# Performance work log

Hardware: AMD Instinct MI355X
Metric: run time of the kernel (lower is better)

Reference implementation:

```python
import jax, jax.numpy as jnp
import numpy as np

TOP_K = 2  # routing_method: renormalize top-2 (topk then softmax over selected logits)


def setup_inputs() -> dict:
    key = jax.random.key(0)
    ks = jax.random.split(key, 5)
    T, H, I, E = 4096, 1024, 4096, 8
    return {
        "hidden_states": jax.random.normal(ks[0], (T, H), jnp.float32),
        "router_logits": jax.random.normal(ks[1], (T, E), jnp.float32),
        "W_gate": jax.random.normal(ks[2], (E, H, I), jnp.float32) * 0.02,  # w1
        "W_up": jax.random.normal(ks[3], (E, H, I), jnp.float32) * 0.02,   # w3
        "W_down": jax.random.normal(ks[4], (E, I, H), jnp.float32) * 0.02, # w2
    }


def reference(hidden_states, router_logits, W_gate, W_up, W_down):
    # Routing: top-k logits, renormalize with softmax over selected logits.
    top_vals, top_idx = jax.lax.top_k(router_logits, TOP_K)        # [T, K]
    routing_weights = jax.nn.softmax(top_vals, axis=-1)            # [T, K]

    E = W_gate.shape[0]
    out = jnp.zeros_like(hidden_states)                            # [T, H]
    for e in range(E):  # fixed small expert loop (structurally distinct weights)
        # combine weight for expert e per token (0 if not routed here)
        w_e = jnp.sum(jnp.where(top_idx == e, routing_weights, 0.0), axis=-1)  # [T]
        gate = hidden_states @ W_gate[e]                           # [T, I]
        up = hidden_states @ W_up[e]                               # [T, I]
        y = (jax.nn.silu(gate) * up) @ W_down[e]                   # [T, H]
        out = out + w_e[:, None] * y
    return out
```

## Files before the change

### kernel.cpp

```cpp
#include <hip/hip_runtime.h>

typedef float    f32x4 __attribute__((ext_vector_type(4)));
typedef _Float16 f16x8 __attribute__((ext_vector_type(8)));
typedef _Float16 f16x4 __attribute__((ext_vector_type(4)));

#define T_TOK 4096
#define HD    1024
#define ID    4096
#define NE    8
#define TOTP  (2*T_TOK)
#define BM    128
#define BN    128
#define MAXTILES 72

#define WS_CNT   0
#define WS_FILL  64
#define WS_OFF   128
#define WS_TOT   192
#define WS_TEXP  256
#define WS_TM0   (256 + 4*MAXTILES)
#define WS_TOPE  1024
#define WS_TOPW  (WS_TOPE + 4*TOTP)
#define WS_PAIR  (WS_TOPW + 4*TOTP)
#define WS_ACT   ((size_t)1 << 20)
constexpr size_t WS_YBUF = WS_ACT  + 2ull*TOTP*ID;
constexpr size_t WS_HS16 = WS_YBUF + 2ull*TOTP*HD;
constexpr size_t WS_WG16 = WS_HS16 + 2ull*T_TOK*HD;
constexpr size_t WS_WU16 = WS_WG16 + 2ull*NE*HD*ID;
constexpr size_t WS_WD16 = WS_WU16 + 2ull*NE*HD*ID;

__device__ __forceinline__ void gll16(const void* g, void* l) {
  __builtin_amdgcn_global_load_lds(
      (const __attribute__((address_space(1))) unsigned int*)g,
      (__attribute__((address_space(3))) unsigned int*)l, 16, 0, 0);
}

#define WAITV(N) do { \
    asm volatile("s_waitcnt vmcnt(" #N ")" ::: "memory"); \
    __builtin_amdgcn_sched_barrier(0); \
  } while (0)

__device__ __forceinline__ int lofs(int row, int g) {
  return row * 32 + ((g ^ ((row >> 1) & 3)) << 3);
}

__global__ void k_router(const float* __restrict__ logits, char* __restrict__ ws) {
  int t = blockIdx.x * blockDim.x + threadIdx.x;
  if (t >= T_TOK) return;
  float v0 = -1e30f, v1 = -1e30f; int i0 = 0, i1 = 0;
  #pragma unroll
  for (int e = 0; e < NE; ++e) {
    float v = logits[t * NE + e];
    if (v > v0)      { v1 = v0; i1 = i0; v0 = v; i0 = e; }
    else if (v > v1) { v1 = v;  i1 = e; }
  }
  float w0 = 1.f / (1.f + __expf(v1 - v0));
  ((int*)(ws + WS_TOPE))[2*t]   = i0;
  ((int*)(ws + WS_TOPE))[2*t+1] = i1;
  ((float*)(ws + WS_TOPW))[2*t]   = w0;
  ((float*)(ws + WS_TOPW))[2*t+1] = 1.f - w0;
  atomicAdd(&((int*)(ws + WS_CNT))[i0], 1);
  atomicAdd(&((int*)(ws + WS_CNT))[i1], 1);
}

__global__ void k_prefix(char* __restrict__ ws) {
  if (threadIdx.x != 0 || blockIdx.x != 0) return;
  const int* cnt = (const int*)(ws + WS_CNT);
  int* off  = (int*)(ws + WS_OFF);
  int* texp = (int*)(ws + WS_TEXP);
  int* tm0  = (int*)(ws + WS_TM0);
  int run = 0, tiles = 0;
  for (int e = 0; e < NE; ++e) {
    off[e] = run;
    int ne = cnt[e];
    for (int i = 0; i < ne; i += BM) { texp[tiles] = e; tm0[tiles] = i; ++tiles; }
    run += ne;
  }
  off[NE] = run;
  *(int*)(ws + WS_TOT) = tiles;
}

__global__ void k_scatter(char* __restrict__ ws) {
  int t = blockIdx.x * blockDim.x + threadIdx.x;
  if (t >= T_TOK) return;
  const int* tope = (const int*)(ws + WS_TOPE);
  const int* off  = (const int*)(ws + WS_OFF);
  int* fill = (int*)(ws + WS_FILL);
  int* pair = (int*)(ws + WS_PAIR);
  #pragma unroll
  for (int s = 0; s < 2; ++s) {
    int id = 2*t + s;
    int e = tope[id];
    int pos = off[e] + atomicAdd(&fill[e], 1);
    pair[pos] = id;
  }
}

__global__ void k_hscvt(const float* __restrict__ src, _Float16* __restrict__ dst) {
  int i = blockIdx.x * blockDim.x + threadIdx.x;
  f32x4 v = ((const f32x4*)src)[i];
  f16x4 o;
  #pragma unroll
  for (int j = 0; j < 4; ++j) o[j] = (_Float16)v[j];
  ((f16x4*)dst)[i] = o;
}

__global__ __launch_bounds__(256) void k_wtrans(const float* __restrict__ src,
                                                _Float16* __restrict__ dst,
                                                int K, int N) {
  const int e = blockIdx.z;
  const int n0 = blockIdx.x * 64, k0 = blockIdx.y * 64;
  const float* s = src + (size_t)e * K * N;
  _Float16* d = dst + (size_t)e * (size_t)K * N;
  __shared__ _Float16 t[64][68];
  const int tx = threadIdx.x & 15, ty = threadIdx.x >> 4;
  #pragma unroll
  for (int it = 0; it < 4; ++it) {
    int k = k0 + it*16 + ty;
    f32x4 v = *(const f32x4*)&s[(size_t)k * N + n0 + tx*4];
    #pragma unroll
    for (int j = 0; j < 4; ++j) t[tx*4 + j][it*16 + ty] = (_Float16)v[j];
  }
  __syncthreads();
  #pragma unroll
  for (int it = 0; it < 4; ++it) {
    int n = it*16 + ty;
    *(f16x4*)&d[(size_t)(n0 + n) * K + k0 + tx*4] = *(const f16x4*)&t[n][tx*4];
  }
}

__global__ __launch_bounds__(512) void k_gemm1(
    const _Float16* __restrict__ hs16, const _Float16* __restrict__ WgT,
    const _Float16* __restrict__ WuT, char* __restrict__ ws) {
  const int s = blockIdx.y;
  if (s >= *(const int*)(ws + WS_TOT)) return;
  const int e    = ((const int*)(ws + WS_TEXP))[s];
  const int m0   = ((const int*)(ws + WS_TM0))[s];
  const int offE = ((const int*)(ws + WS_OFF))[e];
  const int nE   = ((const int*)(ws + WS_CNT))[e];
  _Float16* __restrict__ act = (_Float16*)(ws + WS_ACT);
  const int n0 = blockIdx.x * BN;
  const int tid = threadIdx.x, lane = tid & 63, wid = tid >> 6;

  __shared__ __align__(16) _Float16 sm[3 * 3 * BM * 32];

  const int rL = lane >> 2;
  const int q  = (((lane & 3) ^ ((lane >> 3) & 3)) << 3);
  int tok;
  { int mm = m0 + 16*wid + rL;
    tok = (mm < nE) ? (((const int*)(ws + WS_PAIR))[offE + mm] >> 1) : 0; }
  const _Float16* aS = hs16 + (size_t)tok * HD + q;
  const int colB = n0 + 16*wid + rL;
  const _Float16* gS = WgT + ((size_t)e * ID + colB) * HD + q;
  const _Float16* uS = WuT + ((size_t)e * ID + colB) * HD + q;

  auto stage = [&](int buf, int kt) {
    _Float16* b = sm + buf * (3*BM*32) + wid * 512;
    const int ko = kt * 32;
    gll16(aS + ko, b);
    gll16(gS + ko, b + BM*32);
    gll16(uS + ko, b + 2*BM*32);
  };

  const int wr = wid >> 2, wc = wid & 3;
  const int l15 = lane & 15, l4 = lane >> 4;
  f32x4 accg[4][2] = {}, accu[4][2] = {};

  auto compute = [&](int buf) {
    const _Float16* b0 = sm + buf * (3*BM*32);
    f16x8 afr[4], gfr[2], ufr[2];
    #pragma unroll
    for (int i = 0; i < 4; ++i)
      afr[i] = *(const f16x8*)&b0[lofs(64*wr + 16*i + l15, l4)];
    #pragma unroll
    for (int j = 0; j < 2; ++j) {
      gfr[j] = *(const f16x8*)&b0[BM*32   + lofs(32*wc + 16*j + l15, l4)];
      ufr[j] = *(const f16x8*)&b0[2*BM*32 + lofs(32*wc + 16*j + l15, l4)];
    }
    __builtin_amdgcn_s_setprio(1);
    #pragma unroll
    for (int i = 0; i < 4; ++i)
      #pragma unroll
      for (int j = 0; j < 2; ++j) {
        accg[i][j] = __builtin_amdgcn_mfma_f32_16x16x32_f16(afr[i], gfr[j], accg[i][j], 0, 0, 0);
        accu[i][j] = __builtin_amdgcn_mfma_f32_16x16x32_f16(afr[i], ufr[j], accu[i][j], 0, 0, 0);
      }
    __builtin_amdgcn_s_setprio(0);
  };

  const int KT = HD / 32;
  stage(0, 0); stage(1, 1);
  for (int t = 0; t < KT - 2; ++t) {
    stage((t + 2) % 3, t + 2);
    WAITV(6);
    __builtin_amdgcn_s_barrier();
    compute(t % 3);
    __builtin_amdgcn_s_barrier();
  }
  WAITV(3);
  __builtin_amdgcn_s_barrier();
  compute((KT - 2) % 3);
  __builtin_amdgcn_s_barrier();
  WAITV(0);
  __builtin_amdgcn_s_barrier();
  compute((KT - 1) % 3);

  #pragma unroll
  for (int i = 0; i < 4; ++i)
    #pragma unroll
    for (int r = 0; r < 4; ++r) {
      const int mm = m0 + 64*wr + 16*i + 4*l4 + r;
      if (mm < nE) {
        const size_t prow = (size_t)(offE + mm) * ID;
        #pragma unroll
        for (int j = 0; j < 2; ++j) {
          float g = accg[i][j][r], u = accu[i][j][r];
          float sv = g / (1.f + __expf(-g)) * u;
          act[prow + n0 + 32*wc + 16*j + l15] = (_Float16)sv;
        }
      }
    }
}

__global__ __launch_bounds__(512) void k_gemm2(const _Float16* __restrict__ WdT,
                                               char* __restrict__ ws) {
  const int s = blockIdx.y;
  if (s >= *(const int*)(ws + WS_TOT)) return;
  const int e    = ((const int*)(ws + WS_TEXP))[s];
  const int m0   = ((const int*)(ws + WS_TM0))[s];
  const int offE = ((const int*)(ws + WS_OFF))[e];
  const int nE   = ((const int*)(ws + WS_CNT))[e];
  const int* __restrict__ pair = (const int*)(ws + WS_PAIR);
  const _Float16* __restrict__ act = (const _Float16*)(ws + WS_ACT);
  _Float16* __restrict__ ybuf = (_Float16*)(ws + WS_YBUF);
  const int n0 = blockIdx.x * BN;
  const int tid = threadIdx.x, lane = tid & 63, wid = tid >> 6;

  __shared__ __align__(16) _Float16 sm[3 * 2 * BM * 32];

  const int rL = lane >> 2;
  const int q  = (((lane & 3) ^ ((lane >> 3) & 3)) << 3);
  int pA; { int mm = m0 + 16*wid + rL; pA = (mm < nE) ? (offE + mm) : 0; }
  const _Float16* aS = act + (size_t)pA * ID + q;
  const int cB = n0 + 16*wid + rL;
  const _Float16* bS = WdT + ((size_t)e * HD + cB) * ID + q;

  auto stage = [&](int buf, int kt) {
    _Float16* b = sm + buf * (2*BM*32) + wid * 512;
    const int ko = kt * 32;
    gll16(aS + ko, b);
    gll16(bS + ko, b + BM*32);
  };

  const int wr = wid >> 2, wc = wid & 3;
  const int l15 = lane & 15, l4 = lane >> 4;
  f32x4 acc[4][2] = {};

  auto compute = [&](int buf) {
    const _Float16* b0 = sm + buf * (2*BM*32);
    f16x8 afr[4], bfr[2];
    #pragma unroll
    for (int i = 0; i < 4; ++i)
      afr[i] = *(const f16x8*)&b0[lofs(64*wr + 16*i + l15, l4)];
    #pragma unroll
    for (int j = 0; j < 2; ++j)
      bfr[j] = *(const f16x8*)&b0[BM*32 + lofs(32*wc + 16*j + l15, l4)];
    __builtin_amdgcn_s_setprio(1);
    #pragma unroll
    for (int i = 0; i < 4; ++i)
      #pragma unroll
      for (int j = 0; j < 2; ++j)
        acc[i][j] = __builtin_amdgcn_mfma_f32_16x16x32_f16(afr[i], bfr[j], acc[i][j], 0, 0, 0);
    __builtin_amdgcn_s_setprio(0);
  };

  const int KT = ID / 32;
  stage(0, 0); stage(1, 1);
  for (int t = 0; t < KT - 2; ++t) {
    stage((t + 2) % 3, t + 2);
    WAITV(4);
    __builtin_amdgcn_s_barrier();
    compute(t % 3);
    __builtin_amdgcn_s_barrier();
  }
  WAITV(2);
  __builtin_amdgcn_s_barrier();
  compute((KT - 2) % 3);
  __builtin_amdgcn_s_barrier();
  WAITV(0);
  __builtin_amdgcn_s_barrier();
  compute((KT - 1) % 3);

  #pragma unroll
  for (int i = 0; i < 4; ++i)
    #pragma unroll
    for (int r = 0; r < 4; ++r) {
      const int mm = m0 + 64*wr + 16*i + 4*l4 + r;
      if (mm < nE) {
        const int id = pair[offE + mm];
        #pragma unroll
        for (int j = 0; j < 2; ++j)
          ybuf[(size_t)id * HD + n0 + 32*wc + 16*j + l15] = (_Float16)acc[i][j][r];
      }
    }
}

__global__ void k_combine(const char* __restrict__ ws, float* __restrict__ out) {
  const int idx = blockIdx.x * blockDim.x + threadIdx.x;
  const int t = idx >> 7, c = idx & 127;
  const float* topw = (const float*)(ws + WS_TOPW);
  const _Float16* yb = (const _Float16*)(ws + WS_YBUF);
  f16x8 y0 = ((const f16x8*)(yb + (size_t)(2*t)     * HD))[c];
  f16x8 y1 = ((const f16x8*)(yb + (size_t)(2*t + 1) * HD))[c];
  const float w0 = topw[2*t], w1 = topw[2*t+1];
  f32x4 o0, o1;
  #pragma unroll
  for (int j = 0; j < 4; ++j) {
    o0[j] = w0 * (float)y0[j]     + w1 * (float)y1[j];
    o1[j] = w0 * (float)y0[4 + j] + w1 * (float)y1[4 + j];
  }
  ((f32x4*)out)[2*idx]     = o0;
  ((f32x4*)out)[2*idx + 1] = o1;
}

extern "C" void kernel_launch(void* const* d_in, const int* in_sizes, int n_in,
                              void* d_out, int out_size, void* d_ws, size_t ws_size,
                              hipStream_t stream) {
  const float* hs     = (const float*)d_in[0];
  const float* logits = (const float*)d_in[1];
  const float* Wg     = (const float*)d_in[2];
  const float* Wu     = (const float*)d_in[3];
  const float* Wd     = (const float*)d_in[4];
  char* ws = (char*)d_ws;

  _Float16* hs16 = (_Float16*)(ws + WS_HS16);
  _Float16* wg16 = (_Float16*)(ws + WS_WG16);
  _Float16* wu16 = (_Float16*)(ws + WS_WU16);
  _Float16* wd16 = (_Float16*)(ws + WS_WD16);

  hipMemsetAsync(ws, 0, 256, stream);
  k_router <<<dim3(T_TOK/256), dim3(256), 0, stream>>>(logits, ws);
  k_prefix <<<dim3(1),         dim3(64),  0, stream>>>(ws);
  k_scatter<<<dim3(T_TOK/256), dim3(256), 0, stream>>>(ws);
  k_hscvt  <<<dim3(T_TOK*HD/4/256), dim3(256), 0, stream>>>(hs, hs16);
  k_wtrans <<<dim3(ID/64, HD/64, NE), dim3(256), 0, stream>>>(Wg, wg16, HD, ID);
  k_wtrans <<<dim3(ID/64, HD/64, NE), dim3(256), 0, stream>>>(Wu, wu16, HD, ID);
  k_wtrans <<<dim3(HD/64, ID/64, NE), dim3(256), 0, stream>>>(Wd, wd16, ID, HD);
  k_gemm1  <<<dim3(ID/BN, MAXTILES), dim3(512), 0, stream>>>(hs16, wg16, wu16, ws);
  k_gemm2  <<<dim3(HD/BN, MAXTILES), dim3(512), 0, stream>>>(wd16, ws);
  k_combine<<<dim3(T_TOK*HD/8/256), dim3(256), 0, stream>>>(ws, (float*)d_out);
}
```

Before: 490.3 us.

## Enlarge GEMM block tiles to 128x256 and 256x128 with split staging

The gate/up GEMM now computes a 128x256 output tile per block, processing gate and up sequentially with a shared B-fragment register set. The down GEMM uses 256-row token tiles over 128 columns, with a separate tile list built in the prefix kernel. Each loop iteration issues part of its loads before the barrier and the rest after it, to spread out global-to-LDS traffic. Larger tiles raise arithmetic intensity and cut re-reads of weights and activations, but they use more LDS and registers per block and give fewer blocks for the MoE-sized workload.

```diff
diff --git a/kernel.cpp b/kernel.cpp
--- a/kernel.cpp
+++ b/kernel.cpp
@@ -9,17 +9,19 @@
 #define ID    4096
 #define NE    8
 #define TOTP  (2*T_TOK)
-#define BM    128
-#define BN    128
-#define MAXTILES 72
+#define MAXT1 72
+#define MAXT2 40
 
 #define WS_CNT   0
 #define WS_FILL  64
 #define WS_OFF   128
 #define WS_TOT   192
+#define WS_TOT2  196
 #define WS_TEXP  256
-#define WS_TM0   (256 + 4*MAXTILES)
-#define WS_TOPE  1024
+#define WS_TM0   (256 + 4*MAXT1)
+#define WS_TEXP2 (256 + 8*MAXT1)
+#define WS_TM02  (256 + 8*MAXT1 + 4*MAXT2)
+#define WS_TOPE  2048
 #define WS_TOPW  (WS_TOPE + 4*TOTP)
 #define WS_PAIR  (WS_TOPW + 4*TOTP)
 #define WS_ACT   ((size_t)1 << 20)
@@ -66,18 +68,22 @@
 __global__ void k_prefix(char* __restrict__ ws) {
   if (threadIdx.x != 0 || blockIdx.x != 0) return;
   const int* cnt = (const int*)(ws + WS_CNT);
-  int* off  = (int*)(ws + WS_OFF);
-  int* texp = (int*)(ws + WS_TEXP);
-  int* tm0  = (int*)(ws + WS_TM0);
-  int run = 0, tiles = 0;
+  int* off   = (int*)(ws + WS_OFF);
+  int* texp  = (int*)(ws + WS_TEXP);
+  int* tm0   = (int*)(ws + WS_TM0);
+  int* texp2 = (int*)(ws + WS_TEXP2);
+  int* tm02  = (int*)(ws + WS_TM02);
+  int run = 0, t1 = 0, t2 = 0;
   for (int e = 0; e < NE; ++e) {
     off[e] = run;
     int ne = cnt[e];
-    for (int i = 0; i < ne; i += BM) { texp[tiles] = e; tm0[tiles] = i; ++tiles; }
+    for (int i = 0; i < ne; i += 128) { texp[t1] = e; tm0[t1] = i; ++t1; }
+    for (int i = 0; i < ne; i += 256) { texp2[t2] = e; tm02[t2] = i; ++t2; }
     run += ne;
   }
   off[NE] = run;
-  *(int*)(ws + WS_TOT) = tiles;
+  *(int*)(ws + WS_TOT)  = t1;
+  *(int*)(ws + WS_TOT2) = t2;
 }
 
 __global__ void k_scatter(char* __restrict__ ws) {
@@ -129,6 +135,7 @@
   }
 }
 
+#define G1_BUF 20480
 __global__ __launch_bounds__(512) void k_gemm1(
     const _Float16* __restrict__ hs16, const _Float16* __restrict__ WgT,
     const _Float16* __restrict__ WuT, char* __restrict__ ws) {
@@ -139,65 +146,82 @@
   const int offE = ((const int*)(ws + WS_OFF))[e];
   const int nE   = ((const int*)(ws + WS_CNT))[e];
   _Float16* __restrict__ act = (_Float16*)(ws + WS_ACT);
-  const int n0 = blockIdx.x * BN;
+  const int n0 = blockIdx.x * 256;
   const int tid = threadIdx.x, lane = tid & 63, wid = tid >> 6;
 
-  __shared__ __align__(16) _Float16 sm[3 * 3 * BM * 32];
+  __shared__ __align__(16) _Float16 sm[3 * G1_BUF];
 
   const int rL = lane >> 2;
   const int q  = (((lane & 3) ^ ((lane >> 3) & 3)) << 3);
   int tok;
   { int mm = m0 + 16*wid + rL;
     tok = (mm < nE) ? (((const int*)(ws + WS_PAIR))[offE + mm] >> 1) : 0; }
-  const _Float16* aS = hs16 + (size_t)tok * HD + q;
-  const int colB = n0 + 16*wid + rL;
-  const _Float16* gS = WgT + ((size_t)e * ID + colB) * HD + q;
-  const _Float16* uS = WuT + ((size_t)e * ID + colB) * HD + q;
-
-  auto stage = [&](int buf, int kt) {
-    _Float16* b = sm + buf * (3*BM*32) + wid * 512;
+  const _Float16* aS  = hs16 + (size_t)tok * HD + q;
+  const size_t cB0 = (size_t)e * ID + n0 + 32*wid + rL;
+  const _Float16* gS0 = WgT + cB0 * HD + q;
+  const _Float16* gS1 = gS0 + 16ull * HD;
+  const _Float16* uS0 = WuT + cB0 * HD + q;
+  const _Float16* uS1 = uS0 + 16ull * HD;
+
+  auto stageAG = [&](int buf, int kt) {
+    _Float16* b = sm + buf * G1_BUF;
     const int ko = kt * 32;
-    gll16(aS + ko, b);
-    gll16(gS + ko, b + BM*32);
-    gll16(uS + ko, b + 2*BM*32);
+    gll16(aS  + ko, b + wid*512);
+    gll16(gS0 + ko, b + 4096  + wid*1024);
+    gll16(gS1 + ko, b + 4096  + wid*1024 + 512);
+  };
+  auto stageU = [&](int buf, int kt) {
+    _Float16* b = sm + buf * G1_BUF;
+    const int ko = kt * 32;
+    gll16(uS0 + ko, b + 12288 + wid*1024);
+    gll16(uS1 + ko, b + 12288 + wid*1024 + 512);
   };
 
   const int wr = wid >> 2, wc = wid & 3;
   const int l15 = lane & 15, l4 = lane >> 4;
-  f32x4 accg[4][2] = {}, accu[4][2] = {};
+  f32x4 accg[4][4] = {}, accu[4][4] = {};
 
   auto compute = [&](int buf) {
-    const _Float16* b0 = sm + buf * (3*BM*32);
-    f16x8 afr[4], gfr[2], ufr[2];
+    const _Float16* b0 = sm + buf * G1_BUF;
+    f16x8 afr[4], bfr[4];
     #pragma unroll
     for (int i = 0; i < 4; ++i)
       afr[i] = *(const f16x8*)&b0[lofs(64*wr + 16*i + l15, l4)];
     #pragma unroll
-    for (int j = 0; j < 2; ++j) {
-      gfr[j] = *(const f16x8*)&b0[BM*32   + lofs(32*wc + 16*j + l15, l4)];
-      ufr[j] = *(const f16x8*)&b0[2*BM*32 + lofs(32*wc + 16*j + l15, l4)];
-    }
+    for (int j = 0; j < 4; ++j)
+      bfr[j] = *(const f16x8*)&b0[4096 + lofs(64*wc + 16*j + l15, l4)];
     __builtin_amdgcn_s_setprio(1);
     #pragma unroll
     for (int i = 0; i < 4; ++i)
       #pragma unroll
-      for (int j = 0; j < 2; ++j) {
-        accg[i][j] = __builtin_amdgcn_mfma_f32_16x16x32_f16(afr[i], gfr[j], accg[i][j], 0, 0, 0);
-        accu[i][j] = __builtin_amdgcn_mfma_f32_16x16x32_f16(afr[i], ufr[j], accu[i][j], 0, 0, 0);
-      }
+      for (int j = 0; j < 4; ++j)
+        accg[i][j] = __builtin_amdgcn_mfma_f32_16x16x32_f16(afr[i], bfr[j], accg[i][j], 0, 0, 0);
     __builtin_amdgcn_s_setprio(0);
+    #pragma unroll
+    for (int j = 0; j < 4; ++j)
+      bfr[j] = *(const f16x8*)&b0[12288 + lofs(64*wc + 16*j + l15, l4)];
+    __builtin_amdgcn_s_setprio(1);
+    #pragma unroll
+    for (int i = 0; i < 4; ++i)
+      #pragma unroll
+      for (int j = 0; j < 4; ++j)
+        accu[i][j] = __builtin_amdgcn_mfma_f32_16x16x32_f16(afr[i], bfr[j], accu[i][j], 0, 0, 0);
+    __builtin_amdgcn_s_setprio(0);
   };
 
   const int KT = HD / 32;
-  stage(0, 0); stage(1, 1);
+  stageAG(0, 0); stageU(0, 0);
+  stageAG(1, 1); stageU(1, 1);
   for (int t = 0; t < KT - 2; ++t) {
-    stage((t + 2) % 3, t + 2);
-    WAITV(6);
+    const int nb = (t + 2) % 3;
+    stageAG(nb, t + 2);
+    WAITV(8);
     __builtin_amdgcn_s_barrier();
+    stageU(nb, t + 2);
     compute(t % 3);
     __builtin_amdgcn_s_barrier();
   }
-  WAITV(3);
+  WAITV(5);
   __builtin_amdgcn_s_barrier();
   compute((KT - 2) % 3);
   __builtin_amdgcn_s_barrier();
@@ -213,77 +237,87 @@
       if (mm < nE) {
         const size_t prow = (size_t)(offE + mm) * ID;
         #pragma unroll
-        for (int j = 0; j < 2; ++j) {
+        for (int j = 0; j < 4; ++j) {
           float g = accg[i][j][r], u = accu[i][j][r];
           float sv = g / (1.f + __expf(-g)) * u;
-          act[prow + n0 + 32*wc + 16*j + l15] = (_Float16)sv;
+          act[prow + n0 + 64*wc + 16*j + l15] = (_Float16)sv;
         }
       }
     }
 }
 
+#define G2_BUF 12288
 __global__ __launch_bounds__(512) void k_gemm2(const _Float16* __restrict__ WdT,
                                                char* __restrict__ ws) {
   const int s = blockIdx.y;
-  if (s >= *(const int*)(ws + WS_TOT)) return;
-  const int e    = ((const int*)(ws + WS_TEXP))[s];
-  const int m0   = ((const int*)(ws + WS_TM0))[s];
+  if (s >= *(const int*)(ws + WS_TOT2)) return;
+  const int e    = ((const int*)(ws + WS_TEXP2))[s];
+  const int m0   = ((const int*)(ws + WS_TM02))[s];
   const int offE = ((const int*)(ws + WS_OFF))[e];
   const int nE   = ((const int*)(ws + WS_CNT))[e];
   const int* __restrict__ pair = (const int*)(ws + WS_PAIR);
   const _Float16* __restrict__ act = (const _Float16*)(ws + WS_ACT);
   _Float16* __restrict__ ybuf = (_Float16*)(ws + WS_YBUF);
-  const int n0 = blockIdx.x * BN;
+  const int n0 = blockIdx.x * 128;
   const int tid = threadIdx.x, lane = tid & 63, wid = tid >> 6;
 
-  __shared__ __align__(16) _Float16 sm[3 * 2 * BM * 32];
+  __shared__ __align__(16) _Float16 sm[3 * G2_BUF];
 
   const int rL = lane >> 2;
   const int q  = (((lane & 3) ^ ((lane >> 3) & 3)) << 3);
-  int pA; { int mm = m0 + 16*wid + rL; pA = (mm < nE) ? (offE + mm) : 0; }
-  const _Float16* aS = act + (size_t)pA * ID + q;
-  const int cB = n0 + 16*wid + rL;
-  const _Float16* bS = WdT + ((size_t)e * HD + cB) * ID + q;
-
-  auto stage = [&](int buf, int kt) {
-    _Float16* b = sm + buf * (2*BM*32) + wid * 512;
+  int pA0, pA1;
+  { int mm = m0 + 32*wid + rL;       pA0 = (mm < nE) ? (offE + mm) : offE; }
+  { int mm = m0 + 32*wid + 16 + rL;  pA1 = (mm < nE) ? (offE + mm) : offE; }
+  const _Float16* aS0 = act + (size_t)pA0 * ID + q;
+  const _Float16* aS1 = act + (size_t)pA1 * ID + q;
+  const _Float16* bS  = WdT + ((size_t)e * HD + n0 + 16*wid + rL) * ID + q;
+
+  auto stageBA = [&](int buf, int kt) {
+    _Float16* b = sm + buf * G2_BUF;
     const int ko = kt * 32;
-    gll16(aS + ko, b);
-    gll16(bS + ko, b + BM*32);
-  };
-
-  const int wr = wid >> 2, wc = wid & 3;
+    gll16(bS  + ko, b + 8192 + wid*512);
+    gll16(aS0 + ko, b + wid*1024);
+  };
+  auto stageA1 = [&](int buf, int kt) {
+    _Float16* b = sm + buf * G2_BUF;
+    gll16(aS1 + kt*32, b + wid*1024 + 512);
+  };
+
+  const int wr = wid >> 1, wc = wid & 1;
   const int l15 = lane & 15, l4 = lane >> 4;
-  f32x4 acc[4][2] = {};
+  f32x4 acc[4][4] = {};
 
   auto compute = [&](int buf) {
-    const _Float16* b0 = sm + buf * (2*BM*32);
-    f16x8 afr[4], bfr[2];
+    const _Float16* b0 = sm + buf * G2_BUF;
+    f16x8 afr[4], bfr[4];
     #pragma unroll
     for (int i = 0; i < 4; ++i)
       afr[i] = *(const f16x8*)&b0[lofs(64*wr + 16*i + l15, l4)];
     #pragma unroll
-    for (int j = 0; j < 2; ++j)
-      bfr[j] = *(const f16x8*)&b0[BM*32 + lofs(32*wc + 16*j + l15, l4)];
+    for (int j = 0; j < 4; ++j)
+      bfr[j] = *(const f16x8*)&b0[8192 + lofs(64*wc + 16*j + l15, l4)];
     __builtin_amdgcn_s_setprio(1);
     #pragma unroll
     for (int i = 0; i < 4; ++i)
       #pragma unroll
-      for (int j = 0; j < 2; ++j)
+      for (int j = 0; j < 4; ++j)
         acc[i][j] = __builtin_amdgcn_mfma_f32_16x16x32_f16(afr[i], bfr[j], acc[i][j], 0, 0, 0);
     __builtin_amdgcn_s_setprio(0);
   };
 
   const int KT = ID / 32;
-  stage(0, 0); stage(1, 1);
+  stageBA(0, 0); stageA1(0, 0);
+  stageBA(1, 1); stageA1(1, 1);
   for (int t = 0; t < KT - 2; ++t) {
-    stage((t + 2) % 3, t + 2);
-    WAITV(4);
+    const int nb = (t + 2) % 3;
+    stageBA(nb, t + 2);
+    WAITV(5);
     __builtin_amdgcn_s_barrier();
+    stageA1(nb, t + 2);
     compute(t % 3);
     __builtin_amdgcn_s_barrier();
   }
-  WAITV(2);
+  WAITV(3);
   __builtin_amdgcn_s_barrier();
   compute((KT - 2) % 3);
   __builtin_amdgcn_s_barrier();
@@ -299,8 +333,8 @@
       if (mm < nE) {
         const int id = pair[offE + mm];
         #pragma unroll
-        for (int j = 0; j < 2; ++j)
-          ybuf[(size_t)id * HD + n0 + 32*wc + 16*j + l15] = (_Float16)acc[i][j][r];
+        for (int j = 0; j < 4; ++j)
+          ybuf[(size_t)id * HD + n0 + 64*wc + 16*j + l15] = (_Float16)acc[i][j][r];
       }
     }
 }
@@ -346,7 +380,7 @@
   k_wtrans <<<dim3(ID/64, HD/64, NE), dim3(256), 0, stream>>>(Wg, wg16, HD, ID);
   k_wtrans <<<dim3(ID/64, HD/64, NE), dim3(256), 0, stream>>>(Wu, wu16, HD, ID);
   k_wtrans <<<dim3(HD/64, ID/64, NE), dim3(256), 0, stream>>>(Wd, wd16, ID, HD);
-  k_gemm1  <<<dim3(ID/BN, MAXTILES), dim3(512), 0, stream>>>(hs16, wg16, wu16, ws);
-  k_gemm2  <<<dim3(HD/BN, MAXTILES), dim3(512), 0, stream>>>(wd16, ws);
+  k_gemm1  <<<dim3(ID/256, MAXT1), dim3(512), 0, stream>>>(hs16, wg16, wu16, ws);
+  k_gemm2  <<<dim3(HD/128, MAXT2), dim3(512), 0, stream>>>(wd16, ws);
   k_combine<<<dim3(T_TOK*HD/8/256), dim3(256), 0, stream>>>(ws, (float*)d_out);
 }
```

New measurement: 533.4 us. +8.8%, slower.
